# Kernel tuning notes

Hardware: AMD Instinct MI355X
Metric: run time of the kernel (lower is better)

Reference implementation:

```python
import jax, jax.numpy as jnp
import numpy as np

B, S, D, H = 4, 2048, 2048, 16
HD = D // H            # 128 head dim
HID = 5632             # SwiGLU hidden: multiple_of*ceil((2/3*4*D)/multiple_of)
EPS = 1e-6


def setup_inputs() -> dict:
    key = jax.random.key(0)
    ks = jax.random.split(key, 12)
    s = 0.02
    x = jax.random.normal(ks[0], (B, S, D), dtype=jnp.float32)
    # RoPE freqs (theta=10000), complex freqs_cis represented as cos/sin
    inv_freq = 1.0 / (10000.0 ** (np.arange(0, HD, 2, dtype=np.float32) / HD))
    t = np.arange(S, dtype=np.float32)
    ang = np.outer(t, inv_freq)                      # [S, HD/2]
    freqs_cos = jnp.asarray(np.cos(ang), dtype=jnp.float32)
    freqs_sin = jnp.asarray(np.sin(ang), dtype=jnp.float32)
    # additive causal mask [1,1,S,S]
    mask = jnp.where(jnp.triu(jnp.ones((S, S), dtype=bool), k=1), -jnp.inf, 0.0)
    mask = mask.astype(jnp.float32)[None, None]
    return {
        "x": x,
        "freqs_cos": freqs_cos,
        "freqs_sin": freqs_sin,
        "mask": mask,
        "wq": jax.random.normal(ks[1], (D, D), jnp.float32) * s,
        "wk": jax.random.normal(ks[2], (D, D), jnp.float32) * s,
        "wv": jax.random.normal(ks[3], (D, D), jnp.float32) * s,
        "wo": jax.random.normal(ks[4], (D, D), jnp.float32) * s,
        "w1": jax.random.normal(ks[5], (HID, D), jnp.float32) * s,
        "w2": jax.random.normal(ks[6], (D, HID), jnp.float32) * s,
        "w3": jax.random.normal(ks[7], (HID, D), jnp.float32) * s,
        "attn_norm_w": jnp.ones((D,), jnp.float32),
        "ffn_norm_w": jnp.ones((D,), jnp.float32),
        "start_pos": 0,
    }


def rmsnorm(x, w, eps=EPS):
    xf = x.astype(jnp.float32)
    y = xf * jax.lax.rsqrt(jnp.mean(xf * xf, axis=-1, keepdims=True) + eps)
    return y.astype(x.dtype) * w


def apply_rope(q, k, cos, sin):
    # q,k: [B,S,H,HD]; cos,sin: [S,HD/2]
    def rot(x):
        xf = x.astype(jnp.float32).reshape(*x.shape[:-1], HD // 2, 2)
        xr, xi = xf[..., 0], xf[..., 1]
        c = cos[None, :, None, :]
        s = sin[None, :, None, :]
        out = jnp.stack([xr * c - xi * s, xr * s + xi * c], axis=-1)
        return out.reshape(*x.shape).astype(x.dtype)
    return rot(q), rot(k)


def reference(x, freqs_cos, freqs_sin, mask, wq, wk, wv, wo, w1, w2, w3,
              attn_norm_w, ffn_norm_w, start_pos):
    # ---- attention ----
    xa = rmsnorm(x, attn_norm_w)
    q = (xa @ wq.T).reshape(B, S, H, HD)
    k = (xa @ wk.T).reshape(B, S, H, HD)
    v = (xa @ wv.T).reshape(B, S, H, HD)
    q, k = apply_rope(q, k, freqs_cos, freqs_sin)
    # [B,H,S,S] scores (naive, materialized as in original)
    scores = jnp.einsum('bqhd,bkhd->bhqk', q, k) / jnp.sqrt(jnp.float32(HD))
    scores = scores + mask
    attn = jax.nn.softmax(scores, axis=-1)
    o = jnp.einsum('bhqk,bkhd->bqhd', attn, v).reshape(B, S, D)
    h = x + o @ wo.T
    # ---- SwiGLU FFN ----
    hf = rmsnorm(h, ffn_norm_w)
    ff = (jax.nn.silu(hf @ w1.T) * (hf @ w3.T)) @ w2.T
    return h + ff
```

## Files before the change

kernel.cpp:

```cpp
#include <hip/hip_runtime.h>
#include <hip/hip_bf16.h>
#include <stdint.h>

typedef short  bf16x8_t __attribute__((ext_vector_type(8)));
typedef short  bf16x4_t __attribute__((ext_vector_type(4)));
typedef float  f32x4_t  __attribute__((ext_vector_type(4)));
typedef unsigned short u16;
typedef unsigned int   u32;

#define DEV __device__ __forceinline__

DEV u16 f2bf(float f){
  u32 u = __float_as_uint(f);
  u += 0x7fffu + ((u >> 16) & 1u);
  return (u16)(u >> 16);
}
DEV float bf2f(u16 h){ return __uint_as_float(((u32)h) << 16); }

DEV void gl16(const void* g, void* l){
  __builtin_amdgcn_global_load_lds(
      (const __attribute__((address_space(1))) void*)g,
      (__attribute__((address_space(3))) void*)l, 16, 0, 0);
}

#define SB0() __builtin_amdgcn_sched_barrier(0)
#define BARF() do{ SB0(); __builtin_amdgcn_s_barrier(); SB0(); }while(0)

__global__ __launch_bounds__(256) void cvt_k(const float* __restrict__ in,
                                             u16* __restrict__ out, int n8){
  int i = blockIdx.x * 256 + threadIdx.x;
  if (i >= n8) return;
  const float4* p = (const float4*)in;
  float4 a = p[(size_t)i*2], b = p[(size_t)i*2+1];
  bf16x8_t o;
  o[0]=(short)f2bf(a.x); o[1]=(short)f2bf(a.y); o[2]=(short)f2bf(a.z); o[3]=(short)f2bf(a.w);
  o[4]=(short)f2bf(b.x); o[5]=(short)f2bf(b.y); o[6]=(short)f2bf(b.z); o[7]=(short)f2bf(b.w);
  *(bf16x8_t*)(out + (size_t)i*8) = o;
}

__global__ __launch_bounds__(256) void rmsnorm_k(const float* __restrict__ x,
                                                 const float* __restrict__ w,
                                                 u16* __restrict__ y){
  int row = blockIdx.x, t = threadIdx.x;
  const float4* xr = (const float4*)(x + (size_t)row*2048);
  float4 a = xr[t*2], b = xr[t*2+1];
  float ss = a.x*a.x+a.y*a.y+a.z*a.z+a.w*a.w + b.x*b.x+b.y*b.y+b.z*b.z+b.w*b.w;
  #pragma unroll
  for (int m = 32; m; m >>= 1) ss += __shfl_xor(ss, m, 64);
  __shared__ float red[4];
  if ((t & 63) == 0) red[t >> 6] = ss;
  __syncthreads();
  float tot = red[0]+red[1]+red[2]+red[3];
  float rs = rsqrtf(tot * (1.0f/2048.0f) + 1e-6f);
  const float4* wr = (const float4*)w;
  float4 wa = wr[t*2], wb = wr[t*2+1];
  bf16x8_t o;
  o[0]=(short)f2bf(a.x*rs*wa.x); o[1]=(short)f2bf(a.y*rs*wa.y);
  o[2]=(short)f2bf(a.z*rs*wa.z); o[3]=(short)f2bf(a.w*rs*wa.w);
  o[4]=(short)f2bf(b.x*rs*wb.x); o[5]=(short)f2bf(b.y*rs*wb.y);
  o[6]=(short)f2bf(b.z*rs*wb.z); o[7]=(short)f2bf(b.w*rs*wb.w);
  *(bf16x8_t*)(y + (size_t)row*2048 + t*8) = o;
}

__global__ __launch_bounds__(256) void rmsnorm2_k(const float* __restrict__ x,
                                                  const u16* __restrict__ t1,
                                                  const float* __restrict__ w,
                                                  u16* __restrict__ y){
  int row = blockIdx.x, t = threadIdx.x;
  const float4* xr = (const float4*)(x + (size_t)row*2048);
  float4 a = xr[t*2], b = xr[t*2+1];
  bf16x8_t tv = *(const bf16x8_t*)(t1 + (size_t)row*2048 + t*8);
  float h[8];
  h[0]=a.x+bf2f((u16)tv[0]); h[1]=a.y+bf2f((u16)tv[1]);
  h[2]=a.z+bf2f((u16)tv[2]); h[3]=a.w+bf2f((u16)tv[3]);
  h[4]=b.x+bf2f((u16)tv[4]); h[5]=b.y+bf2f((u16)tv[5]);
  h[6]=b.z+bf2f((u16)tv[6]); h[7]=b.w+bf2f((u16)tv[7]);
  float ss = 0.f;
  #pragma unroll
  for (int j=0;j<8;j++) ss += h[j]*h[j];
  #pragma unroll
  for (int m = 32; m; m >>= 1) ss += __shfl_xor(ss, m, 64);
  __shared__ float red[4];
  if ((t & 63) == 0) red[t >> 6] = ss;
  __syncthreads();
  float tot = red[0]+red[1]+red[2]+red[3];
  float rs = rsqrtf(tot * (1.0f/2048.0f) + 1e-6f);
  const float4* wr = (const float4*)w;
  float4 wa = wr[t*2], wb = wr[t*2+1];
  bf16x8_t o;
  o[0]=(short)f2bf(h[0]*rs*wa.x); o[1]=(short)f2bf(h[1]*rs*wa.y);
  o[2]=(short)f2bf(h[2]*rs*wa.z); o[3]=(short)f2bf(h[3]*rs*wa.w);
  o[4]=(short)f2bf(h[4]*rs*wb.x); o[5]=(short)f2bf(h[5]*rs*wb.y);
  o[6]=(short)f2bf(h[6]*rs*wb.z); o[7]=(short)f2bf(h[7]*rs*wb.w);
  *(bf16x8_t*)(y + (size_t)row*2048 + t*8) = o;
}

__global__ __launch_bounds__(256) void rope_k(u16* __restrict__ q, u16* __restrict__ k,
                                              const float* __restrict__ fc,
                                              const float* __restrict__ fs){
  int i = blockIdx.x * 256 + threadIdx.x;
  int ii = i & 63; int h = (i >> 6) & 15; int bs = i >> 10;
  int s = bs & 2047;
  size_t off = (size_t)bs*2048 + h*128 + 2*ii;
  float c = fc[s*64+ii], sn = fs[s*64+ii];
  u32 qq = *(u32*)(q + off);
  float xr = bf2f((u16)(qq & 0xffff)), xi = bf2f((u16)(qq >> 16));
  *(u32*)(q + off) = (u32)f2bf(xr*c - xi*sn) | ((u32)f2bf(xr*sn + xi*c) << 16);
  u32 kk = *(u32*)(k + off);
  xr = bf2f((u16)(kk & 0xffff)); xi = bf2f((u16)(kk >> 16));
  *(u32*)(k + off) = (u32)f2bf(xr*c - xi*sn) | ((u32)f2bf(xr*sn + xi*c) << 16);
}

__global__ __launch_bounds__(256) void transpose_k(const u16* __restrict__ in,
                                                   u16* __restrict__ out){
  __shared__ u16 tile[64*68];
  int tid = threadIdx.x;
  int tm = blockIdx.x >> 5, tn = blockIdx.x & 31;
  const u16* src = in + (size_t)(tm*64)*2048 + tn*64;
  #pragma unroll
  for (int i=0;i<2;i++){
    int idx = i*256 + tid;
    int r = idx >> 3, c8 = (idx & 7)*8;
    *(bf16x8_t*)&tile[r*68 + c8] = *(const bf16x8_t*)(src + (size_t)r*2048 + c8);
  }
  __syncthreads();
  u16* dst = out + (size_t)(tn*64)*8192 + tm*64;
  #pragma unroll
  for (int i=0;i<2;i++){
    int idx = i*256 + tid;
    int oc = idx >> 3, r8 = (idx & 7)*8;
    bf16x8_t v;
    #pragma unroll
    for (int j=0;j<8;j++) v[j] = tile[(r8+j)*68 + oc];
    *(bf16x8_t*)(dst + (size_t)oc*8192 + r8) = v;
  }
}


DEV void stg(const u16* __restrict__ G, int K, u16* dst, int tid, int Toff){
  #pragma unroll
  for (int j=0;j<2;j++){
    int c = j*512 + tid;
    int row = c >> 2;
    int l = (c&3) ^ ((row>>1)&3);
    gl16(G + (size_t)row*K + Toff + l*8, dst + (size_t)c*8);
  }
}

DEV void rdA(const u16* base, int wm, int mh, int l15, int pc, bf16x8_t (&r)[4]){
  #pragma unroll
  for (int mi=0;mi<4;mi++){
    int R = wm*128 + mh*64 + mi*16 + l15;
    r[mi] = *(const bf16x8_t*)&base[R*32 + pc];
  }
}
DEV void rdB(const u16* base, int wn, int l15, int pc, bf16x8_t (&r)[4]){
  #pragma unroll
  for (int ni=0;ni<4;ni++){
    int R = wn*64 + ni*16 + l15;
    r[ni] = *(const bf16x8_t*)&base[R*32 + pc];
  }
}

template<int MH>
DEV void MM16(bf16x8_t (&a)[4], bf16x8_t (&b)[4], f32x4_t (&acc)[8][4]){
  __builtin_amdgcn_s_setprio(1);
  #pragma unroll
  for (int mi=0;mi<4;mi++)
    #pragma unroll
    for (int ni=0;ni<4;ni++)
      acc[MH*4+mi][ni] =
        __builtin_amdgcn_mfma_f32_16x16x32_bf16(a[mi], b[ni], acc[MH*4+mi][ni], 0,0,0);
  __builtin_amdgcn_s_setprio(0);
}

template<int EPI>
__global__ __launch_bounds__(512, 2) void gemm_bt(const u16* __restrict__ A,
                                                  const u16* __restrict__ B,
                                                  void* __restrict__ C,
                                                  const void* __restrict__ aux,
                                                  const void* __restrict__ aux2,
                                                  int M, int N, int K){
  __shared__ __align__(16) u16 sA[2*2*8192];
  __shared__ __align__(16) u16 sB[2*2*8192];
  int tid = threadIdx.x, lane = tid & 63, wave = tid >> 6;
  int l15 = lane & 15, l4 = lane >> 4;
  int pc = (l4 ^ ((l15 >> 1) & 3)) * 8;
  int nbn = N / 256;
  int nwg = gridDim.x, bid = blockIdx.x;
  int qq = nwg >> 3, rr = nwg & 7;
  int xc = bid & 7, yy = bid >> 3;
  int wg = (xc < rr ? xc*(qq+1) : rr*(qq+1) + (xc-rr)*qq) + yy;
  int tm = wg / nbn, tn = wg % nbn;
  size_t m0 = (size_t)tm*256, n0 = (size_t)tn*256;
  const u16* Ag = A + m0*K;
  const u16* Bg = B + n0*K;
  int wm = wave >> 2, wn = wave & 3;

  f32x4_t acc[8][4];
  #pragma unroll
  for (int i=0;i<8;i++)
    #pragma unroll
    for (int j=0;j<4;j++)
      acc[i][j] = (f32x4_t){0.f,0.f,0.f,0.f};

  int nk = K / 64;
  stg(Ag, K, &sA[0],     tid, 0);  stg(Bg, K, &sB[0],     tid, 0);
  stg(Ag, K, &sA[8192],  tid, 32); stg(Bg, K, &sB[8192],  tid, 32);
  stg(Ag, K, &sA[16384], tid, 64); stg(Bg, K, &sB[16384], tid, 64);
  asm volatile("s_waitcnt vmcnt(8)" ::: "memory");
  BARF();
  bf16x8_t A0[4], A1[4], C0[4], D0[4], B0[4], B1[4];
  rdA(&sA[0], wm, 0, l15, pc, A0);
  rdB(&sB[0], wn, l15, pc, B0);
  rdA(&sA[0], wm, 1, l15, pc, A1);
  SB0();

  for (int T=0; T<nk; ++T){
    int cb = T & 1, nb = cb ^ 1;
    const u16* Ac1 = &sA[cb*16384 + 8192];
    const u16* Bc1 = &sB[cb*16384 + 8192];
    if (T < nk-1) asm volatile("s_waitcnt vmcnt(4)" ::: "memory");
    else          asm volatile("s_waitcnt vmcnt(0)" ::: "memory");
    BARF();
    if (T+1 < nk){
      stg(Ag, K, &sA[nb*16384 + 8192], tid, (T+1)*64 + 32);
      stg(Bg, K, &sB[nb*16384 + 8192], tid, (T+1)*64 + 32);
    }
    SB0();
    rdA(Ac1, wm, 0, l15, pc, C0);
    rdB(Bc1, wn, l15, pc, B1);
    rdA(Ac1, wm, 1, l15, pc, D0);
    SB0();
    MM16<0>(A0, B0, acc);
    MM16<1>(A1, B0, acc);
    MM16<0>(C0, B1, acc);
    if (T < nk-1) asm volatile("s_waitcnt vmcnt(4)" ::: "memory");
    else          asm volatile("s_waitcnt vmcnt(0)" ::: "memory");
    BARF();
    if (T+2 < nk){
      stg(Ag, K, &sA[cb*16384], tid, (T+2)*64);
      stg(Bg, K, &sB[cb*16384], tid, (T+2)*64);
    }
    SB0();
    if (T+1 < nk){
      rdA(&sA[nb*16384], wm, 0, l15, pc, A0);
      rdB(&sB[nb*16384], wn, l15, pc, B0);
      rdA(&sA[nb*16384], wm, 1, l15, pc, A1);
    }
    SB0();
    MM16<1>(D0, B1, acc);
  }

  #pragma unroll
  for (int am=0; am<8; am++)
    #pragma unroll
    for (int ni=0; ni<4; ni++)
      #pragma unroll
      for (int r=0; r<4; r++){
        float v = acc[am][ni][r];
        size_t rowg = m0 + (am&3)*16 + (am>>2)*64 + wm*128 + l4*4 + r;
        size_t colg = n0 + wn*64 + ni*16 + l15;
        size_t idx = rowg * (size_t)N + colg;
        if constexpr (EPI == 0){
          ((u16*)C)[idx] = f2bf(v);
        } else if constexpr (EPI == 1){
          float s = v / (1.0f + __expf(-v));
          ((u16*)C)[idx] = f2bf(s);
        } else if constexpr (EPI == 2){
          float a = bf2f(((const u16*)aux)[idx]);
          ((u16*)C)[idx] = f2bf(v * a);
        } else {
          float a = ((const float*)aux)[idx];
          float b2 = bf2f(((const u16*)aux2)[idx]);
          ((float*)C)[idx] = v + a + b2;
        }
      }
}

__global__ __launch_bounds__(256) void attn_k(const u16* __restrict__ Q,
                                              const u16* __restrict__ K,
                                              const u16* __restrict__ VT,
                                              u16* __restrict__ O){
  __shared__ __align__(16) u16 sK[32*128];
  __shared__ __align__(16) u16 sVT[128*32];
  int tid = threadIdx.x, lane = tid & 63, wave = tid >> 6;
  int bid = blockIdx.x;
  int qt = 31 - (bid >> 6);
  int bh = bid & 63; int b = bh >> 4, h = bh & 15;
  int l15 = lane & 15, l4 = lane >> 4;
  size_t base = ((size_t)b*2048)*2048 + (size_t)h*128;
  const u16* VTg0 = VT + ((size_t)h*128)*8192 + (size_t)b*2048;
  int qr0 = qt*64 + wave*16;
  int qrow = qr0 + l15;
  bf16x8_t qf[4];
  #pragma unroll
  for (int s=0;s<4;s++)
    qf[s] = *(const bf16x8_t*)(Q + base + (size_t)qrow*2048 + s*32 + l4*8);

  f32x4_t oaccT[8];
  #pragma unroll
  for (int f=0;f<8;f++) oaccT[f] = (f32x4_t){0.f,0.f,0.f,0.f};
  float lrun = 0.f;

  const float cl2 = 0.08838834764831845f * 1.4426950408889634f;
  int nkt = (qt + 1) * 2;
  for (int kt=0; kt<nkt; ++kt){
    __syncthreads();
    const u16* Kg = K + base + (size_t)kt*32*2048;
    #pragma unroll
    for (int i=0;i<2;i++){
      int c = i*256 + tid; int row = c>>4;
      gl16(Kg + (size_t)row*2048 + (size_t)(((c&15) ^ (row&7))*8), &sK[c*8]);
    }
    #pragma unroll
    for (int i=0;i<2;i++){
      int c = i*256 + tid; int d = c>>2;
      gl16(VTg0 + (size_t)d*8192 + kt*32 + (size_t)((((c&3) ^ ((d>>1)&3)))*8),
           &sVT[c*8]);
    }
    __syncthreads();

    if (kt*32 <= qr0 + 15){
      f32x4_t sacc[2];
      sacc[0] = (f32x4_t){0.f,0.f,0.f,0.f};
      sacc[1] = (f32x4_t){0.f,0.f,0.f,0.f};
      __builtin_amdgcn_s_setprio(1);
      #pragma unroll
      for (int n=0;n<2;n++)
        #pragma unroll
        for (int s=0;s<4;s++){
          bf16x8_t kf = *(const bf16x8_t*)
              &sK[(n*16 + l15)*128 + (((s*4 + l4) ^ (l15 & 7))*8)];
          sacc[n] = __builtin_amdgcn_mfma_f32_16x16x32_bf16(kf, qf[s], sacc[n], 0,0,0);
        }
      __builtin_amdgcn_s_setprio(0);
      float sum = 0.f;
      bf16x8_t pa;
      bool diag = (kt*32 + 31 > qr0);
      if (diag){
        #pragma unroll
        for (int j=0;j<8;j++){
          int n = j>>2, r = j&3;
          float p = exp2f(sacc[n][r] * cl2);
          int kg = kt*32 + n*16 + l4*4 + r;
          if (kg > qrow) p = 0.f;
          sum += p;
          pa[j] = (short)f2bf(p);
        }
      } else {
        #pragma unroll
        for (int j=0;j<8;j++){
          float p = exp2f(sacc[j>>2][j&3] * cl2);
          sum += p;
          pa[j] = (short)f2bf(p);
        }
      }
      sum += __shfl_xor(sum, 16, 64);
      sum += __shfl_xor(sum, 32, 64);
      lrun += sum;
      __builtin_amdgcn_s_setprio(1);
      #pragma unroll
      for (int f=0;f<8;f++){
        int d = f*16 + l15;
        bf16x4_t lo = *(const bf16x4_t*)&sVT[d*32 + (((0*4 + l4) ^ (d & 6))*4)];
        bf16x4_t hi = *(const bf16x4_t*)&sVT[d*32 + (((1*4 + l4) ^ (d & 6))*4)];
        bf16x8_t va;
        va[0]=lo[0]; va[1]=lo[1]; va[2]=lo[2]; va[3]=lo[3];
        va[4]=hi[0]; va[5]=hi[1]; va[6]=hi[2]; va[7]=hi[3];
        oaccT[f] = __builtin_amdgcn_mfma_f32_16x16x32_bf16(va, pa, oaccT[f], 0,0,0);
      }
      __builtin_amdgcn_s_setprio(0);
    }
  }
  float inv = 1.0f / lrun;
  size_t orow = (size_t)b*2048 + qrow;
  #pragma unroll
  for (int f=0;f<8;f++){
    bf16x4_t ov;
    ov[0]=(short)f2bf(oaccT[f][0]*inv); ov[1]=(short)f2bf(oaccT[f][1]*inv);
    ov[2]=(short)f2bf(oaccT[f][2]*inv); ov[3]=(short)f2bf(oaccT[f][3]*inv);
    *(bf16x4_t*)(O + orow*2048 + h*128 + f*16 + l4*4) = ov;
  }
}

extern "C" void kernel_launch(void* const* d_in, const int* in_sizes, int n_in,
                              void* d_out, int out_size, void* d_ws, size_t ws_size,
                              hipStream_t stream){
  (void)in_sizes; (void)n_in; (void)out_size; (void)ws_size;
  const float* x   = (const float*)d_in[0];
  const float* fc  = (const float*)d_in[1];
  const float* fs  = (const float*)d_in[2];
  const float* wq  = (const float*)d_in[4];
  const float* wk  = (const float*)d_in[5];
  const float* wv  = (const float*)d_in[6];
  const float* wo  = (const float*)d_in[7];
  const float* w1  = (const float*)d_in[8];
  const float* w2  = (const float*)d_in[9];
  const float* w3  = (const float*)d_in[10];
  const float* anw = (const float*)d_in[11];
  const float* fnw = (const float*)d_in[12];
  float* out = (float*)d_out;
  char* ws = (char*)d_ws;

  const int M = 8192, D = 2048, HID = 5632;
  const size_t WB   = 23068672ull;
  const size_t ACT2 = 33554432ull;

  u16* wbuf = (u16*)(ws);
  u16* xa   = (u16*)(ws + WB);
  u16* qb   = (u16*)(ws + WB + ACT2);
  u16* kb   = (u16*)(ws + WB + 2*ACT2);
  u16* vb   = (u16*)(ws + WB + 3*ACT2);
  u16* g1   = (u16*)(ws + WB + 4*ACT2);
  u16* vt = g1;
  u16* t1 = qb;
  u16* hf = kb;

  rmsnorm_k<<<M, 256, 0, stream>>>(x, anw, xa);

  cvt_k<<<D*D/8/256, 256, 0, stream>>>(wq, wbuf, D*D/8);
  gemm_bt<0><<<(M/256)*(D/256), 512, 0, stream>>>(xa, wbuf, qb, nullptr, nullptr, M, D, D);
  cvt_k<<<D*D/8/256, 256, 0, stream>>>(wk, wbuf, D*D/8);
  gemm_bt<0><<<(M/256)*(D/256), 512, 0, stream>>>(xa, wbuf, kb, nullptr, nullptr, M, D, D);
  cvt_k<<<D*D/8/256, 256, 0, stream>>>(wv, wbuf, D*D/8);
  gemm_bt<0><<<(M/256)*(D/256), 512, 0, stream>>>(xa, wbuf, vb, nullptr, nullptr, M, D, D);

  rope_k<<<32768, 256, 0, stream>>>(qb, kb, fc, fs);
  transpose_k<<<4096, 256, 0, stream>>>(vb, vt);

  attn_k<<<2048, 256, 0, stream>>>(qb, kb, vt, xa);

  cvt_k<<<D*D/8/256, 256, 0, stream>>>(wo, wbuf, D*D/8);
  gemm_bt<0><<<(M/256)*(D/256), 512, 0, stream>>>(xa, wbuf, t1, nullptr, nullptr, M, D, D);

  rmsnorm2_k<<<M, 256, 0, stream>>>(x, t1, fnw, hf);

  cvt_k<<<HID*D/8/256, 256, 0, stream>>>(w1, wbuf, HID*D/8);
  gemm_bt<1><<<(M/256)*(HID/256), 512, 0, stream>>>(hf, wbuf, g1, nullptr, nullptr, M, HID, D);
  cvt_k<<<HID*D/8/256, 256, 0, stream>>>(w3, wbuf, HID*D/8);
  gemm_bt<2><<<(M/256)*(HID/256), 512, 0, stream>>>(hf, wbuf, g1, g1, nullptr, M, HID, D);
  cvt_k<<<HID*D/8/256, 256, 0, stream>>>(w2, wbuf, HID*D/8);
  gemm_bt<4><<<(M/256)*(D/256), 512, 0, stream>>>(g1, wbuf, out, x, t1, M, D, HID);
}
```

Measured before the change: 1.294 ms.

## Restructure bf16 GEMM mainloop into 8-phase ping-pong schedule with 128x64 panes

Replaces the two-half-tile double-buffered GEMM mainloop with an 8-phase schedule per pair of K-tiles. Each phase issues one quarter of the LDS reads and one global-to-LDS stage, then runs a 4x2x2 MFMA block between barriers. Shared memory now holds 128x64 panes with an XOR swizzle over 8 chunks, replacing the old 32-wide layout. The goal is finer interleaving of loads and MFMAs and fewer bank conflicts, at the cost of many more workgroup barriers and lgkmcnt(0) waits per iteration. The loop also assumes nk is even.

```diff
diff --git a/kernel.cpp b/kernel.cpp
--- a/kernel.cpp
+++ b/kernel.cpp
@@ -25,6 +25,7 @@
 
 #define SB0() __builtin_amdgcn_sched_barrier(0)
 #define BARF() do{ SB0(); __builtin_amdgcn_s_barrier(); SB0(); }while(0)
+#define LGKM0() do{ asm volatile("s_waitcnt lgkmcnt(0)" ::: "memory"); SB0(); }while(0)
 
 __global__ __launch_bounds__(256) void cvt_k(const float* __restrict__ in,
                                              u16* __restrict__ out, int n8){
@@ -137,40 +138,49 @@
 }
 
 
-DEV void stg(const u16* __restrict__ G, int K, u16* dst, int tid, int Toff){
+DEV void stg(const u16* __restrict__ G, int K, u16* dst, int tid,
+             int rowbase, int Tcol){
   #pragma unroll
   for (int j=0;j<2;j++){
     int c = j*512 + tid;
-    int row = c >> 2;
-    int l = (c&3) ^ ((row>>1)&3);
-    gl16(G + (size_t)row*K + Toff + l*8, dst + (size_t)c*8);
-  }
-}
-
-DEV void rdA(const u16* base, int wm, int mh, int l15, int pc, bf16x8_t (&r)[4]){
-  #pragma unroll
-  for (int mi=0;mi<4;mi++){
-    int R = wm*128 + mh*64 + mi*16 + l15;
-    r[mi] = *(const bf16x8_t*)&base[R*32 + pc];
-  }
-}
-DEV void rdB(const u16* base, int wn, int l15, int pc, bf16x8_t (&r)[4]){
-  #pragma unroll
-  for (int ni=0;ni<4;ni++){
-    int R = wn*64 + ni*16 + l15;
-    r[ni] = *(const bf16x8_t*)&base[R*32 + pc];
-  }
-}
-
-template<int MH>
-DEV void MM16(bf16x8_t (&a)[4], bf16x8_t (&b)[4], f32x4_t (&acc)[8][4]){
+    int row = c >> 3;
+    int lg = (c & 7) ^ (row & 7);
+    gl16(G + (size_t)(rowbase + row)*K + Tcol + lg*8, dst + (size_t)c*8);
+  }
+}
+
+DEV void rdA8(const u16* pane, int mh, int l15, int l4, bf16x8_t (&r)[4][2]){
+  #pragma unroll
+  for (int mi=0;mi<4;mi++)
+    #pragma unroll
+    for (int kk=0;kk<2;kk++){
+      int row = mh*64 + mi*16 + l15;
+      int ch = (kk*4 + l4) ^ (row & 7);
+      r[mi][kk] = *(const bf16x8_t*)&pane[row*64 + ch*8];
+    }
+}
+DEV void rdB4(const u16* pane, int nhl, int wn1, int l15, int l4, bf16x8_t (&r)[2][2]){
+  #pragma unroll
+  for (int nj=0;nj<2;nj++)
+    #pragma unroll
+    for (int kk=0;kk<2;kk++){
+      int row = wn1*64 + (nhl*2+nj)*16 + l15;
+      int ch = (kk*4 + l4) ^ (row & 7);
+      r[nj][kk] = *(const bf16x8_t*)&pane[row*64 + ch*8];
+    }
+}
+
+DEV void MMQ(bf16x8_t (&a)[4][2], bf16x8_t (&b)[2][2], int mh, int nhl,
+             f32x4_t (&acc)[8][4]){
   __builtin_amdgcn_s_setprio(1);
   #pragma unroll
   for (int mi=0;mi<4;mi++)
     #pragma unroll
-    for (int ni=0;ni<4;ni++)
-      acc[MH*4+mi][ni] =
-        __builtin_amdgcn_mfma_f32_16x16x32_bf16(a[mi], b[ni], acc[MH*4+mi][ni], 0,0,0);
+    for (int nj=0;nj<2;nj++)
+      #pragma unroll
+      for (int kk=0;kk<2;kk++)
+        acc[mh*4+mi][nhl*2+nj] = __builtin_amdgcn_mfma_f32_16x16x32_bf16(
+            a[mi][kk], b[nj][kk], acc[mh*4+mi][nhl*2+nj], 0,0,0);
   __builtin_amdgcn_s_setprio(0);
 }
 
@@ -181,11 +191,10 @@
                                                   const void* __restrict__ aux,
                                                   const void* __restrict__ aux2,
                                                   int M, int N, int K){
-  __shared__ __align__(16) u16 sA[2*2*8192];
-  __shared__ __align__(16) u16 sB[2*2*8192];
+  __shared__ __align__(16) u16 sA[2][2][128*64];
+  __shared__ __align__(16) u16 sB[2][2][128*64];
   int tid = threadIdx.x, lane = tid & 63, wave = tid >> 6;
   int l15 = lane & 15, l4 = lane >> 4;
-  int pc = (l4 ^ ((l15 >> 1) & 3)) * 8;
   int nbn = N / 256;
   int nwg = gridDim.x, bid = blockIdx.x;
   int qq = nwg >> 3, rr = nwg & 7;
@@ -196,6 +205,10 @@
   const u16* Ag = A + m0*K;
   const u16* Bg = B + n0*K;
   int wm = wave >> 2, wn = wave & 3;
+  int bh = wn >> 1, wn1 = wn & 1;
+
+  const u16* Ap0 = &sA[0][wm][0];  const u16* Ap1 = &sA[1][wm][0];
+  const u16* Bp0 = &sB[0][bh][0];  const u16* Bp1 = &sB[1][bh][0];
 
   f32x4_t acc[8][4];
   #pragma unroll
@@ -204,52 +217,71 @@
     for (int j=0;j<4;j++)
       acc[i][j] = (f32x4_t){0.f,0.f,0.f,0.f};
 
+  bf16x8_t Ar[4][2], Br0[2][2], Br1[2][2];
   int nk = K / 64;
-  stg(Ag, K, &sA[0],     tid, 0);  stg(Bg, K, &sB[0],     tid, 0);
-  stg(Ag, K, &sA[8192],  tid, 32); stg(Bg, K, &sB[8192],  tid, 32);
-  stg(Ag, K, &sA[16384], tid, 64); stg(Bg, K, &sB[16384], tid, 64);
-  asm volatile("s_waitcnt vmcnt(8)" ::: "memory");
+
+  stg(Ag, K, &sA[0][0][0], tid, 0,   0);
+  stg(Ag, K, &sA[0][1][0], tid, 128, 0);
+  stg(Bg, K, &sB[0][0][0], tid, 0,   0);
+  stg(Bg, K, &sB[0][1][0], tid, 128, 0);
+  stg(Bg, K, &sB[1][0][0], tid, 0,   64);
+  stg(Bg, K, &sB[1][1][0], tid, 128, 64);
+  asm volatile("s_waitcnt vmcnt(4)" ::: "memory");
   BARF();
-  bf16x8_t A0[4], A1[4], C0[4], D0[4], B0[4], B1[4];
-  rdA(&sA[0], wm, 0, l15, pc, A0);
-  rdB(&sB[0], wn, l15, pc, B0);
-  rdA(&sA[0], wm, 1, l15, pc, A1);
-  SB0();
-
-  for (int T=0; T<nk; ++T){
-    int cb = T & 1, nb = cb ^ 1;
-    const u16* Ac1 = &sA[cb*16384 + 8192];
-    const u16* Bc1 = &sB[cb*16384 + 8192];
-    if (T < nk-1) asm volatile("s_waitcnt vmcnt(4)" ::: "memory");
-    else          asm volatile("s_waitcnt vmcnt(0)" ::: "memory");
-    BARF();
-    if (T+1 < nk){
-      stg(Ag, K, &sA[nb*16384 + 8192], tid, (T+1)*64 + 32);
-      stg(Bg, K, &sB[nb*16384 + 8192], tid, (T+1)*64 + 32);
-    }
-    SB0();
-    rdA(Ac1, wm, 0, l15, pc, C0);
-    rdB(Bc1, wn, l15, pc, B1);
-    rdA(Ac1, wm, 1, l15, pc, D0);
-    SB0();
-    MM16<0>(A0, B0, acc);
-    MM16<1>(A1, B0, acc);
-    MM16<0>(C0, B1, acc);
-    if (T < nk-1) asm volatile("s_waitcnt vmcnt(4)" ::: "memory");
-    else          asm volatile("s_waitcnt vmcnt(0)" ::: "memory");
-    BARF();
-    if (T+2 < nk){
-      stg(Ag, K, &sA[cb*16384], tid, (T+2)*64);
-      stg(Bg, K, &sB[cb*16384], tid, (T+2)*64);
-    }
-    SB0();
-    if (T+1 < nk){
-      rdA(&sA[nb*16384], wm, 0, l15, pc, A0);
-      rdB(&sB[nb*16384], wn, l15, pc, B0);
-      rdA(&sA[nb*16384], wm, 1, l15, pc, A1);
-    }
-    SB0();
-    MM16<1>(D0, B1, acc);
+
+  for (int i=0; i<nk/2; ++i){
+    int T0 = 2*i;
+    bool s2 = (T0+2 < nk), s3 = (T0+3 < nk);
+    rdA8(Ap0, 0, l15, l4, Ar);
+    rdB4(Bp0, 0, wn1, l15, l4, Br0);
+    stg(Ag, K, &sA[1][0][0], tid, 0, (T0+1)*64);
+    BARF(); LGKM0();
+    MMQ(Ar, Br0, 0, 0, acc);
+    BARF();
+    rdB4(Bp0, 1, wn1, l15, l4, Br1);
+    stg(Ag, K, &sA[1][1][0], tid, 128, (T0+1)*64);
+    BARF(); LGKM0();
+    MMQ(Ar, Br1, 0, 1, acc);
+    BARF();
+    rdA8(Ap0, 1, l15, l4, Ar);
+    if (s2) stg(Bg, K, &sB[0][0][0], tid, 0, (T0+2)*64);
+    BARF(); LGKM0();
+    MMQ(Ar, Br0, 1, 0, acc);
+    BARF();
+    if (s2){
+      stg(Bg, K, &sB[0][1][0], tid, 128, (T0+2)*64);
+      asm volatile("s_waitcnt vmcnt(4)" ::: "memory");
+    } else {
+      asm volatile("s_waitcnt vmcnt(0)" ::: "memory");
+    }
+    BARF(); LGKM0();
+    MMQ(Ar, Br1, 1, 1, acc);
+    BARF();
+    rdA8(Ap1, 0, l15, l4, Ar);
+    rdB4(Bp1, 0, wn1, l15, l4, Br0);
+    if (s2) stg(Ag, K, &sA[0][0][0], tid, 0, (T0+2)*64);
+    BARF(); LGKM0();
+    MMQ(Ar, Br0, 0, 0, acc);
+    BARF();
+    rdB4(Bp1, 1, wn1, l15, l4, Br1);
+    if (s2) stg(Ag, K, &sA[0][1][0], tid, 128, (T0+2)*64);
+    BARF(); LGKM0();
+    MMQ(Ar, Br1, 0, 1, acc);
+    BARF();
+    rdA8(Ap1, 1, l15, l4, Ar);
+    if (s3) stg(Bg, K, &sB[1][0][0], tid, 0, (T0+3)*64);
+    BARF(); LGKM0();
+    MMQ(Ar, Br0, 1, 0, acc);
+    BARF();
+    if (s3){
+      stg(Bg, K, &sB[1][1][0], tid, 128, (T0+3)*64);
+      asm volatile("s_waitcnt vmcnt(4)" ::: "memory");
+    } else {
+      asm volatile("s_waitcnt vmcnt(0)" ::: "memory");
+    }
+    BARF(); LGKM0();
+    MMQ(Ar, Br1, 1, 1, acc);
+    BARF();
   }
 
   #pragma unroll
```

Measured after the change: 1.138 ms. 1.14x faster.
